# Kernel optimization log

Hardware: AMD Instinct MI355X
Metric: run time of the kernel (lower is better)

The kernel has to match this reference:

```python
import jax, jax.numpy as jnp
import numpy as np

B, S, HID, HEADS = 8, 1024, 1024, 16
DK = HID // HEADS


def setup_inputs() -> dict:
    key = jax.random.key(0)
    ks = jax.random.split(key, 6)
    scale = 1.0 / np.sqrt(HID)
    return {
        "q": jax.random.normal(ks[0], (B, S, HID), jnp.float32),
        "k": jax.random.normal(ks[1], (B, S, HID), jnp.float32),
        "v": jax.random.normal(ks[2], (B, S, HID), jnp.float32),
        "Wq": jax.random.normal(ks[3], (HID, HID), jnp.float32) * scale,
        "Wk": jax.random.normal(ks[4], (HID, HID), jnp.float32) * scale,
        "Wv": jax.random.normal(ks[5], (HID, HID), jnp.float32) * scale,
        "mask": 1,
    }


def _split_heads(x):
    # [B, S, HID] -> [B, HEADS, S, DK]
    b, s, _ = x.shape
    return x.reshape(b, s, HEADS, DK).transpose(0, 2, 1, 3)


def reference(q, k, v, Wq, Wk, Wv, mask):
    # torch nn.Linear: y = x @ W.T (no bias)
    qh = _split_heads(q @ Wq.T)
    kh = _split_heads(k @ Wk.T)
    vh = _split_heads(v @ Wv.T)

    scores = jnp.einsum("bhqd,bhkd->bhqk", qh, kh) / jnp.sqrt(jnp.asarray(DK, qh.dtype))
    scores = jax.nn.softmax(scores, axis=-1)
    if mask:
        # original zeroes entries where row > col AFTER softmax (keeps upper triangle)
        tri = jnp.triu(jnp.ones((S, S), scores.dtype))
        scores = scores * tri
        # original then transposes the (masked) score matrix before applying to V
        scores = scores.transpose(0, 1, 3, 2)
    out = jnp.einsum("bhqk,bhkd->bhqd", scores, vh)
    # [B, HEADS, S, DK] -> [B, S, HID]
    return out.transpose(0, 2, 1, 3).reshape(q.shape[0], -1, HID)
```

## Files before the change

kernel.cpp:

```cpp
#include <hip/hip_runtime.h>
#include <math.h>

#define B 8
#define S 1024
#define HID 1024
#define HEADS 16
#define DK 64

typedef unsigned short u16;
typedef unsigned int u32;
typedef _Float16 f16;
typedef __attribute__((ext_vector_type(8))) _Float16 half8;
typedef __attribute__((ext_vector_type(4))) _Float16 half4;
typedef __attribute__((ext_vector_type(2))) _Float16 half2;
typedef __attribute__((ext_vector_type(2))) __fp16 fp16x2;
typedef __attribute__((ext_vector_type(4))) float f32x4;

#define GLL16(G, L)                                                         \
    __builtin_amdgcn_global_load_lds(                                       \
        (const __attribute__((address_space(1))) u32*)(G),                  \
        (__attribute__((address_space(3))) u32*)(L), 16, 0, 0)

__device__ __forceinline__ float exp_s(float c) {
#if __has_builtin(__builtin_amdgcn_exp2f)
    return __builtin_amdgcn_exp2f(c * 0.18033688f);
#else
    return __expf(c * 0.125f);
#endif
}

__global__ __launch_bounds__(256) void cast_all(
    const float* __restrict__ q, const float* __restrict__ k,
    const float* __restrict__ v, const float* __restrict__ Wq,
    const float* __restrict__ Wk, const float* __restrict__ Wv,
    f16* __restrict__ oq, f16* __restrict__ ok, f16* __restrict__ ov,
    f16* __restrict__ owq, f16* __restrict__ owk, f16* __restrict__ owv) {
    const size_t SZ = (size_t)B * S * HID;
    const size_t WZ = (size_t)HID * HID;
    size_t e = ((size_t)blockIdx.x * 256 + threadIdx.x) * 8;
    const float* src;
    f16* dst;
    if (e < SZ)               { src = q + e;               dst = oq + e; }
    else if (e < 2 * SZ)      { src = k + (e - SZ);        dst = ok + (e - SZ); }
    else if (e < 3 * SZ)      { src = v + (e - 2 * SZ);    dst = ov + (e - 2 * SZ); }
    else if (e < 3 * SZ + WZ) { src = Wq + (e - 3 * SZ);   dst = owq + (e - 3 * SZ); }
    else if (e < 3 * SZ + 2 * WZ) { src = Wk + (e - 3 * SZ - WZ); dst = owk + (e - 3 * SZ - WZ); }
    else                      { src = Wv + (e - 3 * SZ - 2 * WZ); dst = owv + (e - 3 * SZ - 2 * WZ); }
    f32x4 a = *(const f32x4*)src;
    f32x4 b = *(const f32x4*)(src + 4);
    half8 h;
    h[0] = (f16)a[0]; h[1] = (f16)a[1]; h[2] = (f16)a[2]; h[3] = (f16)a[3];
    h[4] = (f16)b[0]; h[5] = (f16)b[1]; h[6] = (f16)b[2]; h[7] = (f16)b[3];
    *(half8*)dst = h;
}

__global__ __launch_bounds__(256) void proj_mfma_b(
    const f16* __restrict__ Xq, const f16* __restrict__ Xk,
    const f16* __restrict__ Xv, const f16* __restrict__ Wq,
    const f16* __restrict__ Wk, const f16* __restrict__ Wv,
    f16* __restrict__ Qb, f16* __restrict__ Kb, f16* __restrict__ Vt) {
    const int L = blockIdx.x;
    const int xcd = L & 7;
    const int w8 = L >> 3;
    const int cx = w8 & 7;
    const int g = xcd * 24 + (w8 >> 3);
    const int z = g % 3;
    const int ytile = g / 3;

    const f16* __restrict__ X = (z == 0) ? Xq : (z == 1) ? Xk : Xv;
    const f16* __restrict__ W = (z == 0) ? Wq : (z == 1) ? Wk : Wv;

    __shared__ u16 As[128 * 32];
    __shared__ u16 Bs[128 * 32];
    const int tid = threadIdx.x;
    const int wv = tid >> 6, ln = tid & 63;
    const int lr = ln & 15, quad = ln >> 4;
    const int wm = wv >> 1, wn = wv & 1;
    const int row0 = ytile * 128, col0 = cx * 128;

    const int srow = tid >> 2;
    const int sch = tid & 3;

    f32x4 acc[4][4];
    #pragma unroll
    for (int i = 0; i < 4; ++i)
        #pragma unroll
        for (int j = 0; j < 4; ++j) acc[i][j] = (f32x4){0.f, 0.f, 0.f, 0.f};

    for (int k0 = 0; k0 < HID; k0 += 32) {
        #pragma unroll
        for (int p = 0; p < 2; ++p) {
            int r = p * 64 + srow;
            int csw = sch ^ ((r >> 1) & 3);
            GLL16(X + (size_t)(row0 + r) * HID + k0 + csw * 8, As + p * 2048 + tid * 8);
            GLL16(W + (size_t)(col0 + r) * HID + k0 + csw * 8, Bs + p * 2048 + tid * 8);
        }
        __syncthreads();
        half8 a[4], b[4];
        #pragma unroll
        for (int mi = 0; mi < 4; ++mi) {
            int r = wm * 64 + mi * 16 + lr;
            a[mi] = *(const half8*)(As + r * 32 + ((quad ^ ((r >> 1) & 3)) * 8));
        }
        #pragma unroll
        for (int ni = 0; ni < 4; ++ni) {
            int r = wn * 64 + ni * 16 + lr;
            b[ni] = *(const half8*)(Bs + r * 32 + ((quad ^ ((r >> 1) & 3)) * 8));
        }
        #pragma unroll
        for (int mi = 0; mi < 4; ++mi)
            #pragma unroll
            for (int ni = 0; ni < 4; ++ni)
                acc[mi][ni] = __builtin_amdgcn_mfma_f32_16x16x32_f16(
                    a[mi], b[ni], acc[mi][ni], 0, 0, 0);
        __syncthreads();
    }

    if (z < 2) {
        f16* __restrict__ Y = (z == 0) ? Qb : Kb;
        #pragma unroll
        for (int mi = 0; mi < 4; ++mi) {
            int m = row0 + wm * 64 + mi * 16 + quad * 4;
            #pragma unroll
            for (int ni = 0; ni < 4; ++ni) {
                int n = col0 + wn * 64 + ni * 16 + lr;
                #pragma unroll
                for (int r = 0; r < 4; ++r)
                    Y[(size_t)(m + r) * HID + n] = (f16)acc[mi][ni][r];
            }
        }
    } else {
        #pragma unroll
        for (int mi = 0; mi < 4; ++mi) {
            int m = row0 + wm * 64 + mi * 16 + quad * 4;
            int bb = m >> 10, s = m & 1023;
            #pragma unroll
            for (int ni = 0; ni < 4; ++ni) {
                int n = col0 + wn * 64 + ni * 16 + lr;
                half4 h4;
                #pragma unroll
                for (int r = 0; r < 4; ++r) h4[r] = (f16)acc[mi][ni][r];
                *(half4*)(Vt + ((size_t)(bb * 16 + (n >> 6)) * 64 + (n & 63)) * S + s) = h4;
            }
        }
    }
}

__global__ __launch_bounds__(256) void stats_mfma(const f16* __restrict__ Q,
                                                  const f16* __restrict__ K,
                                                  f16* __restrict__ Vt) {
    const int bh = blockIdx.x, jt = blockIdx.y;
    const int b = bh >> 4, h = bh & 15;
    const int tid = threadIdx.x;
    const int wv = tid >> 6, ln = tid & 63;
    const int lr = ln & 15, quad = ln >> 4;
    __shared__ u16 Ks[64 * 64];
    __shared__ float rlL[128];

    half8 aq[2][2];
    #pragma unroll
    for (int jsub = 0; jsub < 2; ++jsub) {
        const int j = jt * 128 + wv * 32 + jsub * 16 + lr;
        const f16* qrow = Q + (size_t)(b * S + j) * HID + h * 64;
        aq[jsub][0] = *(const half8*)(qrow + quad * 8);
        aq[jsub][1] = *(const half8*)(qrow + 32 + quad * 8);
    }

    float sl[2][4] = {};

    for (int i0 = 0; i0 < S; i0 += 64) {
        __syncthreads();
        #pragma unroll
        for (int p = 0; p < 2; ++p) {
            int r = p * 32 + (tid >> 3);
            int csw = (tid & 7) ^ (r & 7);
            GLL16(K + (size_t)(b * S + i0 + r) * HID + h * 64 + csw * 8,
                  Ks + p * 2048 + tid * 8);
        }
        __syncthreads();
        #pragma unroll
        for (int isub = 0; isub < 4; ++isub) {
            int il = isub * 16 + lr;
            half8 bk0 = *(const half8*)(Ks + il * 64 + (((0 + quad) ^ (il & 7)) * 8));
            half8 bk1 = *(const half8*)(Ks + il * 64 + (((4 + quad) ^ (il & 7)) * 8));
            #pragma unroll
            for (int jsub = 0; jsub < 2; ++jsub) {
                f32x4 c = {0.f, 0.f, 0.f, 0.f};
                c = __builtin_amdgcn_mfma_f32_16x16x32_f16(aq[jsub][0], bk0, c, 0, 0, 0);
                c = __builtin_amdgcn_mfma_f32_16x16x32_f16(aq[jsub][1], bk1, c, 0, 0, 0);
                #pragma unroll
                for (int r = 0; r < 4; ++r) sl[jsub][r] += exp_s(c[r]);
            }
        }
    }

    #pragma unroll
    for (int jsub = 0; jsub < 2; ++jsub)
        #pragma unroll
        for (int r = 0; r < 4; ++r) {
            float v = sl[jsub][r];
            v += __shfl_xor(v, 1, 64);
            v += __shfl_xor(v, 2, 64);
            v += __shfl_xor(v, 4, 64);
            v += __shfl_xor(v, 8, 64);
            if (lr == 0) rlL[wv * 32 + jsub * 16 + quad * 4 + r] = 1.0f / v;
        }
    __syncthreads();

    {
        const int d = tid >> 2, cg = (tid & 3) * 32;
        f16* vrow = Vt + (size_t)(bh * 64 + d) * S + jt * 128 + cg;
        #pragma unroll
        for (int c8 = 0; c8 < 4; ++c8) {
            half8 hv = *(half8*)(vrow + c8 * 8);
            #pragma unroll
            for (int e = 0; e < 8; ++e)
                hv[e] = (f16)((float)hv[e] * rlL[cg + c8 * 8 + e]);
            *(half8*)(vrow + c8 * 8) = hv;
        }
    }
}

__global__ __launch_bounds__(256) void apply_mfma(const f16* __restrict__ Q,
                                                  const f16* __restrict__ K,
                                                  const f16* __restrict__ Vt,
                                                  float* __restrict__ out) {
    const int bh = blockIdx.x;
    const int it2 = (gridDim.y - 1) - blockIdx.y;
    const int b = bh >> 4, h = bh & 15;
    const int tid = threadIdx.x;
    const int wv = tid >> 6, ln = tid & 63;
    const int lr = ln & 15, quad = ln >> 4;
    const int i0b = it2 * 128;
    const int i0w = i0b + wv * 32;

    __shared__ u16 Qs[64 * 64];
    __shared__ u16 Vts[64 * 64];

    half8 bk[2][2];
    #pragma unroll
    for (int isub = 0; isub < 2; ++isub) {
        int i = i0w + isub * 16 + lr;
        #pragma unroll
        for (int kf = 0; kf < 2; ++kf)
            bk[isub][kf] = *(const half8*)(K + (size_t)(b * S + i) * HID + h * 64 +
                                           kf * 32 + quad * 8);
    }

    f32x4 acc[4][2];
    #pragma unroll
    for (int nt = 0; nt < 4; ++nt)
        #pragma unroll
        for (int isub = 0; isub < 2; ++isub) acc[nt][isub] = (f32x4){0.f, 0.f, 0.f, 0.f};

    const int nch = 2 * it2 + 2;
    for (int jc = 0; jc < nch; ++jc) {
        const int j0 = jc * 64;
        __syncthreads();
        #pragma unroll
        for (int p = 0; p < 2; ++p) {
            int r = p * 32 + (tid >> 3);
            int csw = (tid & 7) ^ (r & 7);
            GLL16(Q + (size_t)(b * S + j0 + r) * HID + h * 64 + csw * 8,
                  Qs + p * 2048 + tid * 8);
        }
        #pragma unroll
        for (int p = 0; p < 2; ++p) {
            int d = p * 32 + (tid >> 3);
            int csw = (tid & 7) ^ (d & 7);
            GLL16(Vt + (size_t)(bh * 64 + d) * S + j0 + csw * 8,
                  Vts + p * 2048 + tid * 8);
        }
        __syncthreads();

        #pragma unroll
        for (int jsub = 0; jsub < 4; ++jsub) {
            const int jbase = j0 + jsub * 16;
            if (jbase > i0w + 31) break;

            const int jl = jsub * 16 + lr;
            half8 aq0 = *(const half8*)(Qs + jl * 64 + (((0 + quad) ^ (jl & 7)) * 8));
            half8 aq1 = *(const half8*)(Qs + jl * 64 + (((4 + quad) ^ (jl & 7)) * 8));
            half4 av[4];
            #pragma unroll
            for (int nt = 0; nt < 4; ++nt) {
                int d = nt * 16 + lr;
                int ch = (jsub * 2 + (quad >> 1)) ^ (d & 7);
                av[nt] = *(const half4*)(Vts + d * 64 + ch * 8 + (quad & 1) * 4);
            }

            #pragma unroll
            for (int isub = 0; isub < 2; ++isub) {
                const int ib = i0w + isub * 16;
                if (jbase > ib + 15) continue;
                f32x4 c = {0.f, 0.f, 0.f, 0.f};
                c = __builtin_amdgcn_mfma_f32_16x16x32_f16(aq0, bk[isub][0], c, 0, 0, 0);
                c = __builtin_amdgcn_mfma_f32_16x16x32_f16(aq1, bk[isub][1], c, 0, 0, 0);
                float w0 = exp_s(c[0]), w1 = exp_s(c[1]);
                float w2 = exp_s(c[2]), w3 = exp_s(c[3]);
                if (jbase + 15 > ib) {
                    const int i_col = ib + lr;
                    const int jq = jbase + quad * 4;
                    if (jq + 0 > i_col) w0 = 0.f;
                    if (jq + 1 > i_col) w1 = 0.f;
                    if (jq + 2 > i_col) w2 = 0.f;
                    if (jq + 3 > i_col) w3 = 0.f;
                }
                fp16x2 q0 = __builtin_amdgcn_cvt_pkrtz(w0, w1);
                fp16x2 q1 = __builtin_amdgcn_cvt_pkrtz(w2, w3);
                half2 p0 = __builtin_bit_cast(half2, q0);
                half2 p1 = __builtin_bit_cast(half2, q1);
                half4 bw;
                bw[0] = p0[0]; bw[1] = p0[1]; bw[2] = p1[0]; bw[3] = p1[1];
                #pragma unroll
                for (int nt = 0; nt < 4; ++nt)
                    acc[nt][isub] = __builtin_amdgcn_mfma_f32_16x16x16f16(
                        av[nt], bw, acc[nt][isub], 0, 0, 0);
            }
        }
    }

    #pragma unroll
    for (int isub = 0; isub < 2; ++isub) {
        int i = i0w + isub * 16 + lr;
        #pragma unroll
        for (int nt = 0; nt < 4; ++nt)
            *(f32x4*)(out + (size_t)(b * S + i) * HID + h * 64 + nt * 16 + quad * 4) =
                acc[nt][isub];
    }
}

extern "C" void kernel_launch(void* const* d_in, const int* in_sizes, int n_in,
                              void* d_out, int out_size, void* d_ws, size_t ws_size,
                              hipStream_t stream) {
    const float* q  = (const float*)d_in[0];
    const float* k  = (const float*)d_in[1];
    const float* v  = (const float*)d_in[2];
    const float* Wq = (const float*)d_in[3];
    const float* Wk = (const float*)d_in[4];
    const float* Wv = (const float*)d_in[5];

    const size_t SZ = (size_t)B * S * HID;
    const size_t WZ = (size_t)HID * HID;

    f16* xq = (f16*)d_out;
    f16* xk = xq + SZ;

    char* p = (char*)d_ws;
    f16* xv = (f16*)p;      p += SZ * 2;
    f16* wq = (f16*)p;      p += WZ * 2;
    f16* wk = (f16*)p;      p += WZ * 2;
    f16* wv_ = (f16*)p;     p += WZ * 2;
    f16* Qb = (f16*)p;      p += SZ * 2;
    f16* Kb = (f16*)p;      p += SZ * 2;
    f16* Vt = (f16*)p;      p += SZ * 2;

    float* out = (float*)d_out;

    const int ncast = (int)((3 * SZ + 3 * WZ) / 8 / 256);
    cast_all<<<ncast, 256, 0, stream>>>(q, k, v, Wq, Wk, Wv,
                                        xq, xk, xv, wq, wk, wv_);

    proj_mfma_b<<<1536, 256, 0, stream>>>(xq, xk, xv, wq, wk, wv_, Qb, Kb, Vt);

    stats_mfma<<<dim3(B * HEADS, S / 128), 256, 0, stream>>>(Qb, Kb, Vt);
    apply_mfma<<<dim3(B * HEADS, S / 128), 256, 0, stream>>>(Qb, Kb, Vt, out);
}
```

Before: 297.8 us.

## Double-buffer K and Q/V LDS tiles and fold softmax scale into Q

The stats and apply attention kernels now double-buffer their shared-memory tiles. The next K tile (or Q/Vt tile) is issued with global_load_lds right after the single barrier, so the fetch overlaps compute on the current tile and one barrier per iteration goes away. The 1/sqrt(dk)·log2(e) factor is applied once when the projection kernel writes Q, so exp_s becomes a bare exp2 with no per-element multiply. The Vt normalisation pass is reindexed so neighbouring threads touch neighbouring 8-element chunks, for better coalescing. The cost is twice the LDS per block, which may lower occupancy, plus a slight fp16 rounding difference from scaling Q before the cast.

```diff
diff --git a/kernel.cpp b/kernel.cpp
--- a/kernel.cpp
+++ b/kernel.cpp
@@ -23,9 +23,9 @@
 
 __device__ __forceinline__ float exp_s(float c) {
 #if __has_builtin(__builtin_amdgcn_exp2f)
-    return __builtin_amdgcn_exp2f(c * 0.18033688f);
+    return __builtin_amdgcn_exp2f(c);
 #else
-    return __expf(c * 0.125f);
+    return exp2f(c);
 #endif
 }
 
@@ -118,6 +118,7 @@
 
     if (z < 2) {
         f16* __restrict__ Y = (z == 0) ? Qb : Kb;
+        const float sc = (z == 0) ? 0.18033688f : 1.0f;
         #pragma unroll
         for (int mi = 0; mi < 4; ++mi) {
             int m = row0 + wm * 64 + mi * 16 + quad * 4;
@@ -126,7 +127,7 @@
                 int n = col0 + wn * 64 + ni * 16 + lr;
                 #pragma unroll
                 for (int r = 0; r < 4; ++r)
-                    Y[(size_t)(m + r) * HID + n] = (f16)acc[mi][ni][r];
+                    Y[(size_t)(m + r) * HID + n] = (f16)(acc[mi][ni][r] * sc);
             }
         }
     } else {
@@ -154,8 +155,20 @@
     const int tid = threadIdx.x;
     const int wv = tid >> 6, ln = tid & 63;
     const int lr = ln & 15, quad = ln >> 4;
-    __shared__ u16 Ks[64 * 64];
+    __shared__ u16 Ks[2][64 * 64];
     __shared__ float rlL[128];
+
+    auto stageK = [&](int bufi, int i0v) {
+        #pragma unroll
+        for (int p = 0; p < 2; ++p) {
+            int r = p * 32 + (tid >> 3);
+            int csw = (tid & 7) ^ (r & 7);
+            GLL16(K + (size_t)(b * S + i0v + r) * HID + h * 64 + csw * 8,
+                  Ks[bufi] + p * 2048 + tid * 8);
+        }
+    };
+
+    stageK(0, 0);
 
     half8 aq[2][2];
     #pragma unroll
@@ -168,21 +181,15 @@
 
     float sl[2][4] = {};
 
-    for (int i0 = 0; i0 < S; i0 += 64) {
+    for (int t = 0; t < S / 64; ++t) {
         __syncthreads();
-        #pragma unroll
-        for (int p = 0; p < 2; ++p) {
-            int r = p * 32 + (tid >> 3);
-            int csw = (tid & 7) ^ (r & 7);
-            GLL16(K + (size_t)(b * S + i0 + r) * HID + h * 64 + csw * 8,
-                  Ks + p * 2048 + tid * 8);
-        }
-        __syncthreads();
+        if (t + 1 < S / 64) stageK((t + 1) & 1, (t + 1) * 64);
+        const u16* Kst = Ks[t & 1];
         #pragma unroll
         for (int isub = 0; isub < 4; ++isub) {
             int il = isub * 16 + lr;
-            half8 bk0 = *(const half8*)(Ks + il * 64 + (((0 + quad) ^ (il & 7)) * 8));
-            half8 bk1 = *(const half8*)(Ks + il * 64 + (((4 + quad) ^ (il & 7)) * 8));
+            half8 bk0 = *(const half8*)(Kst + il * 64 + (((0 + quad) ^ (il & 7)) * 8));
+            half8 bk1 = *(const half8*)(Kst + il * 64 + (((4 + quad) ^ (il & 7)) * 8));
             #pragma unroll
             for (int jsub = 0; jsub < 2; ++jsub) {
                 f32x4 c = {0.f, 0.f, 0.f, 0.f};
@@ -208,15 +215,16 @@
     __syncthreads();
 
     {
-        const int d = tid >> 2, cg = (tid & 3) * 32;
-        f16* vrow = Vt + (size_t)(bh * 64 + d) * S + jt * 128 + cg;
-        #pragma unroll
-        for (int c8 = 0; c8 < 4; ++c8) {
-            half8 hv = *(half8*)(vrow + c8 * 8);
+        const int d = tid >> 2, lc = (tid & 3) * 8;
+        f16* vrow = Vt + (size_t)(bh * 64 + d) * S + jt * 128;
+        #pragma unroll
+        for (int g = 0; g < 4; ++g) {
+            const int c0 = g * 32 + lc;
+            half8 hv = *(half8*)(vrow + c0);
             #pragma unroll
             for (int e = 0; e < 8; ++e)
-                hv[e] = (f16)((float)hv[e] * rlL[cg + c8 * 8 + e]);
-            *(half8*)(vrow + c8 * 8) = hv;
+                hv[e] = (f16)((float)hv[e] * rlL[c0 + e]);
+            *(half8*)(vrow + c0) = hv;
         }
     }
 }
@@ -234,8 +242,27 @@
     const int i0b = it2 * 128;
     const int i0w = i0b + wv * 32;
 
-    __shared__ u16 Qs[64 * 64];
-    __shared__ u16 Vts[64 * 64];
+    __shared__ u16 Qs[2][64 * 64];
+    __shared__ u16 Vts[2][64 * 64];
+
+    auto stageQV = [&](int bufi, int j0v) {
+        #pragma unroll
+        for (int p = 0; p < 2; ++p) {
+            int r = p * 32 + (tid >> 3);
+            int csw = (tid & 7) ^ (r & 7);
+            GLL16(Q + (size_t)(b * S + j0v + r) * HID + h * 64 + csw * 8,
+                  Qs[bufi] + p * 2048 + tid * 8);
+        }
+        #pragma unroll
+        for (int p = 0; p < 2; ++p) {
+            int d = p * 32 + (tid >> 3);
+            int csw = (tid & 7) ^ (d & 7);
+            GLL16(Vt + (size_t)(bh * 64 + d) * S + j0v + csw * 8,
+                  Vts[bufi] + p * 2048 + tid * 8);
+        }
+    };
+
+    stageQV(0, 0);
 
     half8 bk[2][2];
     #pragma unroll
@@ -257,21 +284,9 @@
     for (int jc = 0; jc < nch; ++jc) {
         const int j0 = jc * 64;
         __syncthreads();
-        #pragma unroll
-        for (int p = 0; p < 2; ++p) {
-            int r = p * 32 + (tid >> 3);
-            int csw = (tid & 7) ^ (r & 7);
-            GLL16(Q + (size_t)(b * S + j0 + r) * HID + h * 64 + csw * 8,
-                  Qs + p * 2048 + tid * 8);
-        }
-        #pragma unroll
-        for (int p = 0; p < 2; ++p) {
-            int d = p * 32 + (tid >> 3);
-            int csw = (tid & 7) ^ (d & 7);
-            GLL16(Vt + (size_t)(bh * 64 + d) * S + j0 + csw * 8,
-                  Vts + p * 2048 + tid * 8);
-        }
-        __syncthreads();
+        if (jc + 1 < nch) stageQV((jc + 1) & 1, j0 + 64);
+        const u16* Qsc = Qs[jc & 1];
+        const u16* Vsc = Vts[jc & 1];
 
         #pragma unroll
         for (int jsub = 0; jsub < 4; ++jsub) {
@@ -279,14 +294,14 @@
             if (jbase > i0w + 31) break;
 
             const int jl = jsub * 16 + lr;
-            half8 aq0 = *(const half8*)(Qs + jl * 64 + (((0 + quad) ^ (jl & 7)) * 8));
-            half8 aq1 = *(const half8*)(Qs + jl * 64 + (((4 + quad) ^ (jl & 7)) * 8));
+            half8 aq0 = *(const half8*)(Qsc + jl * 64 + (((0 + quad) ^ (jl & 7)) * 8));
+            half8 aq1 = *(const half8*)(Qsc + jl * 64 + (((4 + quad) ^ (jl & 7)) * 8));
             half4 av[4];
             #pragma unroll
             for (int nt = 0; nt < 4; ++nt) {
                 int d = nt * 16 + lr;
                 int ch = (jsub * 2 + (quad >> 1)) ^ (d & 7);
-                av[nt] = *(const half4*)(Vts + d * 64 + ch * 8 + (quad & 1) * 4);
+                av[nt] = *(const half4*)(Vsc + d * 64 + ch * 8 + (quad & 1) * 4);
             }
 
             #pragma unroll
```

After: 285.3 us. 1.04x faster.
